# Kernel optimization log

Hardware: AMD Instinct MI355X
Metric: run time of the kernel (lower is better)

## Reference

```python
import jax, jax.numpy as jnp
import numpy as np

BN_EPS = 1e-3      # Keras BatchNormalization default epsilon
LRELU_ALPHA = 0.3  # Keras LeakyReLU default alpha


def _bn(x, gamma, beta, mean, var):
    # inference-mode batch norm over the feature (last) axis
    return gamma * (x - mean) * jax.lax.rsqrt(var + BN_EPS) + beta


def _gcn(x, adj, w, b):
    # spektral GCNConv: A_hat @ (X @ W) + b   (adj assumed pre-normalized)
    xw = jnp.einsum('bnf,fc->bnc', x, w)
    return jnp.einsum('bnm,bmc->bnc', adj, xw) + b


def _lrelu(x):
    return jnp.where(x >= 0, x, LRELU_ALPHA * x)


def setup_inputs() -> dict:
    key = jax.random.key(0)
    ks = jax.random.split(key, 12)
    B, N, C = 16, 1024, 256
    x = jax.random.normal(ks[0], (B, N, C), dtype=jnp.float32)
    # roughly row-normalized dense adjacency (stands in for D^-1/2 (A+I) D^-1/2)
    adj = jax.random.uniform(ks[1], (B, N, N), dtype=jnp.float32) / N
    s = 1.0 / np.sqrt(C)
    return {
        'x': x,
        'adj': adj,
        'bn1_gamma': jnp.ones((C,), jnp.float32),
        'bn1_beta': jnp.zeros((C,), jnp.float32),
        'bn1_mean': jax.random.normal(ks[2], (C,), jnp.float32) * 0.1,
        'bn1_var': jax.random.uniform(ks[3], (C,), jnp.float32) + 0.5,
        'w1': jax.random.normal(ks[4], (C, C), jnp.float32) * s,
        'b1': jnp.zeros((C,), jnp.float32),
        'bn2_gamma': jnp.ones((C,), jnp.float32),
        'bn2_beta': jnp.zeros((C,), jnp.float32),
        'bn2_mean': jax.random.normal(ks[5], (C,), jnp.float32) * 0.1,
        'bn2_var': jax.random.uniform(ks[6], (C,), jnp.float32) + 0.5,
        'w2': jax.random.normal(ks[7], (C, C), jnp.float32) * s,
        'b2': jnp.zeros((C,), jnp.float32),
        'w_skip': jax.random.normal(ks[8], (C, C), jnp.float32) * s,
        'b_skip': jnp.zeros((C,), jnp.float32),
    }


def reference(x, adj, bn1_gamma, bn1_beta, bn1_mean, bn1_var, w1, b1,
              bn2_gamma, bn2_beta, bn2_mean, bn2_var, w2, b2, w_skip, b_skip):
    h = _bn(x, bn1_gamma, bn1_beta, bn1_mean, bn1_var)          # BN(input)
    out = _lrelu(_gcn(h, adj, w1, b1))                          # GCNConv + LeakyReLU
    out = _bn(out, bn2_gamma, bn2_beta, bn2_mean, bn2_var)      # BN
    out = _lrelu(_gcn(out, adj, w2, b2))                        # GCNConv + LeakyReLU
    skip = _gcn(h, adj, w_skip, b_skip)                         # skip GCNConv on BN(input)
    # Dropout is identity at inference
    return out + skip
```

## Files before the change

kernel.cpp:

```cpp
#include <hip/hip_runtime.h>

#define LRELU_ALPHA 0.3f
#define BN_EPS 1e-3f

using u16 = unsigned short;
using u32 = unsigned int;

typedef __attribute__((ext_vector_type(8))) short bf16x8;
typedef __attribute__((ext_vector_type(4))) float f32x4;

struct alignas(8) U16x4 { u16 x, y, z, w; };

__device__ __forceinline__ u16 f2bf(float f) {
  union { float f; u32 u; } v; v.f = f;
  u32 b = v.u;
  b += 0x7FFFu + ((b >> 16) & 1u);
  return (u16)(b >> 16);
}
__device__ __forceinline__ float bf2f(u16 h) {
  union { u32 u; float f; } v; v.u = ((u32)h) << 16;
  return v.f;
}

typedef const __attribute__((address_space(1))) void* gas_ptr;
typedef __attribute__((address_space(3))) void* las_ptr;

__device__ __forceinline__ void gload16(const void* g, void* l) {
  __builtin_amdgcn_global_load_lds((gas_ptr)g, (las_ptr)l, 16, 0, 0);
}

__device__ __forceinline__ int xcd_swz512(int lid) {
  return (lid & 7) * 64 + (lid >> 3);
}

template <int K>
__device__ __forceinline__ void gemm_core(const u16* __restrict__ A,
                                          const u16* __restrict__ B,
                                          u16* lds, f32x4 (&acc)[4][4]) {
  const int t = threadIdx.x, lane = t & 63, wid = t >> 6;
  const int wm = (wid >> 1) * 64, wn = (wid & 1) * 64;
  const int lrow = lane & 15, lk = (lane >> 4) * 8;
  const int r0 = t >> 3, ce = (t & 7) * 8, lo = wid * 512;
  u16* ldsA = lds;
  u16* ldsB = lds + 8192;
#pragma unroll 1
  for (int kt = 0; kt < K / 64; ++kt) {
    const u16* gA = A + kt * 64;
    const u16* gB = B + kt * 64;
#pragma unroll
    for (int cc = 0; cc < 4; ++cc) {
      gload16(gA + (size_t)(cc * 32 + r0) * K + ce, ldsA + cc * 2048 + lo);
      gload16(gB + (size_t)(cc * 32 + r0) * K + ce, ldsB + cc * 2048 + lo);
    }
    asm volatile("s_waitcnt vmcnt(0)" ::: "memory");
    __syncthreads();
#pragma unroll
    for (int kk = 0; kk < 2; ++kk) {
      bf16x8 a[4], b[4];
#pragma unroll
      for (int i = 0; i < 4; ++i)
        a[i] = *(const bf16x8*)(ldsA + (wm + i * 16 + lrow) * 64 + kk * 32 + lk);
#pragma unroll
      for (int i = 0; i < 4; ++i)
        b[i] = *(const bf16x8*)(ldsB + (wn + i * 16 + lrow) * 64 + kk * 32 + lk);
#pragma unroll
      for (int i = 0; i < 4; ++i)
#pragma unroll
        for (int j = 0; j < 4; ++j)
          acc[i][j] = __builtin_amdgcn_mfma_f32_16x16x32_bf16(a[i], b[j], acc[i][j], 0, 0, 0);
    }
    __syncthreads();
  }
}

template <int K>
__device__ __forceinline__ void gemm_core64(const u16* __restrict__ A,
                                            const u16* __restrict__ B,
                                            u16* lds, f32x4 (&acc)[2][4]) {
  const int t = threadIdx.x, lane = t & 63, wid = t >> 6;
  const int wm = wid * 32;
  const int lrow = lane & 15, lk = (lane >> 4) * 8;
  const int r0 = t >> 3, ce = (t & 7) * 8, lo = wid * 512;
  u16* ldsA = lds;
  u16* ldsB = lds + 8192;
#pragma unroll 1
  for (int kt = 0; kt < K / 64; ++kt) {
    const u16* gA = A + kt * 64;
    const u16* gB = B + kt * 64;
#pragma unroll
    for (int cc = 0; cc < 4; ++cc)
      gload16(gA + (size_t)(cc * 32 + r0) * K + ce, ldsA + cc * 2048 + lo);
#pragma unroll
    for (int cc = 0; cc < 2; ++cc)
      gload16(gB + (size_t)(cc * 32 + r0) * K + ce, ldsB + cc * 2048 + lo);
    asm volatile("s_waitcnt vmcnt(0)" ::: "memory");
    __syncthreads();
#pragma unroll
    for (int kk = 0; kk < 2; ++kk) {
      bf16x8 a[2], b[4];
#pragma unroll
      for (int i = 0; i < 2; ++i)
        a[i] = *(const bf16x8*)(ldsA + (wm + i * 16 + lrow) * 64 + kk * 32 + lk);
#pragma unroll
      for (int j = 0; j < 4; ++j)
        b[j] = *(const bf16x8*)(ldsB + (j * 16 + lrow) * 64 + kk * 32 + lk);
#pragma unroll
      for (int i = 0; i < 2; ++i)
#pragma unroll
        for (int j = 0; j < 4; ++j)
          acc[i][j] = __builtin_amdgcn_mfma_f32_16x16x32_bf16(a[i], b[j], acc[i][j], 0, 0, 0);
    }
    __syncthreads();
  }
}

#define ACC_INIT(R)                                 \
  f32x4 acc[R][4];                                  \
  _Pragma("unroll") for (int i_ = 0; i_ < R; ++i_)  \
  _Pragma("unroll") for (int j_ = 0; j_ < 4; ++j_)  \
      acc[i_][j_] = {0.f, 0.f, 0.f, 0.f};

__global__ __launch_bounds__(256) void k_prep_h(
    const float* __restrict__ w1, const float* __restrict__ wsk, const float* __restrict__ w2,
    const float* __restrict__ g1, const float* __restrict__ be1,
    const float* __restrict__ m1, const float* __restrict__ v1,
    const float* __restrict__ g2, const float* __restrict__ be2,
    const float* __restrict__ m2, const float* __restrict__ v2,
    const float* __restrict__ x,
    u16* __restrict__ wcatT, u16* __restrict__ w2T,
    float* __restrict__ s2, float* __restrict__ t2c, u16* __restrict__ h_bf) {
  int bid = blockIdx.x;
  if (bid < 768) {
    if (bid == 0) {
      int c = threadIdx.x;
      float a2 = g2[c] * rsqrtf(v2[c] + BN_EPS);
      s2[c] = a2;
      t2c[c] = be2[c] - m2[c] * a2;
    }
    int i = bid * 256 + threadIdx.x;
    if (i < 131072) {
      int co = i >> 8, ci = i & 255;
      const float* w = (co < 256) ? w1 : wsk;
      wcatT[i] = f2bf(w[ci * 256 + (co & 255)]);
    } else {
      int k = i - 131072;
      int co = k >> 8, ci = k & 255;
      w2T[k] = f2bf(w2[ci * 256 + co]);
    }
  } else {
    int base = (bid - 768) * 256 + threadIdx.x;
    int c0 = (base << 2) & 255;
    float sc[4], sh[4];
#pragma unroll
    for (int u = 0; u < 4; ++u) {
      int c = c0 + u;
      float a = g1[c] * rsqrtf(v1[c] + BN_EPS);
      sc[u] = a;
      sh[u] = be1[c] - m1[c] * a;
    }
#pragma unroll
    for (int j = 0; j < 16; ++j) {
      int k = j * 65536 + base;
      float4 v = ((const float4*)x)[k];
      U16x4 o = {f2bf(v.x * sc[0] + sh[0]), f2bf(v.y * sc[1] + sh[1]),
                 f2bf(v.z * sc[2] + sh[2]), f2bf(v.w * sc[3] + sh[3])};
      ((U16x4*)h_bf)[k] = o;
    }
  }
}

__global__ __launch_bounds__(256) void k_cvt(const float* __restrict__ adj,
                                             u16* __restrict__ adj_bf) {
  const int N4 = 4194304;
  int stride = gridDim.x * blockDim.x;
  for (int idx = blockIdx.x * blockDim.x + threadIdx.x; idx < N4; idx += stride) {
    float4 v = ((const float4*)adj)[idx];
    U16x4 o = {f2bf(v.x), f2bf(v.y), f2bf(v.z), f2bf(v.w)};
    ((U16x4*)adj_bf)[idx] = o;
  }
}

__global__ __launch_bounds__(256) void k_xw(const u16* __restrict__ h_bf,
                                            const u16* __restrict__ wcatT,
                                            u16* __restrict__ hwT) {
  __shared__ u16 lds[17408];
  const int wg = xcd_swz512(blockIdx.x);
  const int mt = wg >> 2, nt = wg & 3;
  ACC_INIT(4);
  gemm_core<256>(h_bf + (size_t)mt * 128 * 256, wcatT + (size_t)nt * 128 * 256, lds, acc);

  const int t = threadIdx.x, lane = t & 63, wid = t >> 6;
  const int row0 = (wid >> 1) * 64 + (lane >> 4) * 4;
  const int col0 = (wid & 1) * 64 + (lane & 15);
  __syncthreads();
  u16* tl = lds;
#pragma unroll
  for (int j = 0; j < 4; ++j) {
    int co_l = col0 + j * 16;
#pragma unroll
    for (int i = 0; i < 4; ++i)
#pragma unroll
      for (int q = 0; q < 4; ++q)
        tl[co_l * 136 + row0 + i * 16 + q] = f2bf(acc[i][j][q]);
  }
  __syncthreads();
  const int rw = t >> 4, seg = t & 15;
  const int b = mt >> 3, nb = (mt & 7) * 128;
#pragma unroll
  for (int p = 0; p < 8; ++p) {
    int co_l = p * 16 + rw;
    *(bf16x8*)(hwT + (((size_t)(b * 512 + nt * 128 + co_l)) << 10) + nb + seg * 8) =
        *(const bf16x8*)(tl + co_l * 136 + seg * 8);
  }
}

__global__ __launch_bounds__(256) void k_big1(const u16* __restrict__ adj_bf,
                                              const u16* __restrict__ hwT,
                                              const float* __restrict__ b1,
                                              const float* __restrict__ bsk,
                                              const float* __restrict__ s2,
                                              const float* __restrict__ t2c,
                                              u16* __restrict__ u2b,
                                              u16* __restrict__ skipb) {
  __shared__ u16 lds[17408];
  ACC_INIT(4);
  const int wg = xcd_swz512(blockIdx.x);
  const int mt = wg & 7, nt = (wg >> 3) & 3, bz = wg >> 5;
  gemm_core<1024>(adj_bf + ((size_t)bz << 20) + (size_t)mt * 128 * 1024,
                  hwT    + ((size_t)bz << 19) + (size_t)nt * 128 * 1024, lds, acc);

  const int t = threadIdx.x, lane = t & 63, wid = t >> 6;
  const int row0 = (wid >> 1) * 64 + (lane >> 4) * 4;
  const int col0 = (wid & 1) * 64 + (lane & 15);
  const bool conv = (nt < 2);
  const int cb = (nt & 1) * 128;
  __syncthreads();
  u16* tl = lds;
#pragma unroll
  for (int j = 0; j < 4; ++j) {
    int cl = col0 + j * 16;
    int c = cb + cl;
    float bias = conv ? b1[c] : bsk[c];
    float sc = s2[c], tc = t2c[c];
#pragma unroll
    for (int i = 0; i < 4; ++i)
#pragma unroll
      for (int q = 0; q < 4; ++q) {
        float y = acc[i][j][q] + bias;
        float v;
        if (conv) {
          float u = (y >= 0.f) ? y : LRELU_ALPHA * y;
          v = fmaf(u, sc, tc);
        } else {
          v = y;
        }
        tl[(row0 + i * 16 + q) * 136 + cl] = f2bf(v);
      }
  }
  __syncthreads();
  u16* dstbase = (conv ? u2b : skipb) + ((size_t)bz << 18) + cb;
  const int rw = t >> 4, seg = t & 15;
  const int nb = mt * 128;
#pragma unroll
  for (int p = 0; p < 8; ++p) {
    int nl = p * 16 + rw;
    *(bf16x8*)(dstbase + ((size_t)(nb + nl) << 8) + seg * 8) =
        *(const bf16x8*)(tl + nl * 136 + seg * 8);
  }
}

__global__ __launch_bounds__(256) void k_sm2(const u16* __restrict__ w2T,
                                             const u16* __restrict__ u2b,
                                             u16* __restrict__ t2T) {
  __shared__ u16 lds[12288];
  ACC_INIT(2);
  const int mt = blockIdx.x, nt = blockIdx.y, bz = blockIdx.z;
  gemm_core64<256>(w2T + (size_t)mt * 128 * 256,
                   u2b + ((size_t)bz << 18) + (size_t)nt * 64 * 256, lds, acc);

  const int t = threadIdx.x, lane = t & 63, wid = t >> 6;
  const int row0 = wid * 32 + (lane >> 4) * 4;
  const int col0 = lane & 15;
  __syncthreads();
  u16* tl = lds;
#pragma unroll
  for (int j = 0; j < 4; ++j)
#pragma unroll
    for (int i = 0; i < 2; ++i)
#pragma unroll
      for (int q = 0; q < 4; ++q)
        tl[(row0 + i * 16 + q) * 72 + col0 + j * 16] = f2bf(acc[i][j][q]);
  __syncthreads();
  u16* base = t2T + ((size_t)bz << 18) + nt * 64;
  const int rw = t >> 3, seg = t & 7;
#pragma unroll
  for (int p = 0; p < 4; ++p) {
    int co = p * 32 + rw;
    *(bf16x8*)(base + (((size_t)(mt * 128 + co)) << 10) + seg * 8) =
        *(const bf16x8*)(tl + co * 72 + seg * 8);
  }
}

__global__ __launch_bounds__(256) void k_big2(const u16* __restrict__ adj_bf,
                                              const u16* __restrict__ t2T,
                                              const float* __restrict__ b2,
                                              const u16* __restrict__ skipb,
                                              float* __restrict__ outp) {
  __shared__ u16 lds[17408];
  ACC_INIT(2);
  const int wg = xcd_swz512(blockIdx.x);
  const int mt = wg & 7, nt = (wg >> 3) & 3, bz = wg >> 5;
  gemm_core64<1024>(adj_bf + ((size_t)bz << 20) + (size_t)mt * 128 * 1024,
                    t2T    + ((size_t)bz << 18) + (size_t)nt * 64 * 1024, lds, acc);

  const int t = threadIdx.x, lane = t & 63, wid = t >> 6;
  const int row0 = wid * 32 + (lane >> 4) * 4;
  const int col0 = lane & 15;
  __syncthreads();
  float* tf = (float*)lds;
#pragma unroll
  for (int j = 0; j < 4; ++j) {
    int cl = col0 + j * 16;
    float bias = b2[nt * 64 + cl];
#pragma unroll
    for (int i = 0; i < 2; ++i)
#pragma unroll
      for (int q = 0; q < 4; ++q) {
        float y = acc[i][j][q] + bias;
        tf[(row0 + i * 16 + q) * 68 + cl] = (y >= 0.f) ? y : LRELU_ALPHA * y;
      }
  }
  __syncthreads();
  const int rw = t >> 4, seg = t & 15;
#pragma unroll
  for (int p = 0; p < 8; ++p) {
    int nl = p * 16 + rw;
    size_t go = ((size_t)bz << 18) + ((size_t)(mt * 128 + nl) << 8) + nt * 64 + seg * 4;
    float4 v = *(const float4*)(tf + nl * 68 + seg * 4);
    U16x4 sk = *(const U16x4*)(skipb + go);
    float4 o = {v.x + bf2f(sk.x), v.y + bf2f(sk.y), v.z + bf2f(sk.z), v.w + bf2f(sk.w)};
    *(float4*)(outp + go) = o;
  }
}

extern "C" void kernel_launch(void* const* d_in, const int* in_sizes, int n_in,
                              void* d_out, int out_size, void* d_ws, size_t ws_size,
                              hipStream_t stream) {
  const float* x   = (const float*)d_in[0];
  const float* adj = (const float*)d_in[1];
  const float* g1  = (const float*)d_in[2];
  const float* be1 = (const float*)d_in[3];
  const float* mu1 = (const float*)d_in[4];
  const float* v1  = (const float*)d_in[5];
  const float* w1  = (const float*)d_in[6];
  const float* b1  = (const float*)d_in[7];
  const float* g2  = (const float*)d_in[8];
  const float* be2 = (const float*)d_in[9];
  const float* mu2 = (const float*)d_in[10];
  const float* v2  = (const float*)d_in[11];
  const float* w2  = (const float*)d_in[12];
  const float* b2  = (const float*)d_in[13];
  const float* wsk = (const float*)d_in[14];
  const float* bsk = (const float*)d_in[15];
  float* out = (float*)d_out;

  char* ws = (char*)d_ws;
  u16*   adj_bf = (u16*)(ws);
  u16*   hwT    = (u16*)(ws + 33554432);
  u16*   h_bf   = (u16*)(ws + 50331648);
  u16*   u2b    = (u16*)(ws + 58720256);
  u16*   t2T    = (u16*)(ws + 67108864);
  u16*   skipb  = (u16*)(ws + 75497472);
  u16*   wcatT  = (u16*)(ws + 83886080);
  u16*   w2T    = (u16*)(ws + 84148224);
  float* s2     = (float*)(ws + 84281344);
  float* t2c    = (float*)(ws + 84282368);
  if (ws_size < 84283392) return;

  k_prep_h <<<1024, 256, 0, stream>>>(w1, wsk, w2, g1, be1, mu1, v1, g2, be2, mu2, v2,
                                      x, wcatT, w2T, s2, t2c, h_bf);
  k_cvt    <<<2048, 256, 0, stream>>>(adj, adj_bf);
  k_xw     <<<512,  256, 0, stream>>>(h_bf, wcatT, hwT);
  k_big1   <<<512,  256, 0, stream>>>(adj_bf, hwT, b1, bsk, s2, t2c, u2b, skipb);
  k_sm2 <<<dim3(2, 16, 16), 256, 0, stream>>>(w2T, u2b, t2T);
  k_big2   <<<512,  256, 0, stream>>>(adj_bf, t2T, b2, skipb, out);
}
```

Baseline: 210.7 us.

## Move skip GCN aggregation into second adjacency GEMM and merge conversion kernels

The skip branch's adjacency product is removed from k_big1, which now computes only the conv half with 64-wide tiles. It is instead computed inside k_big2 through a dual-B GEMM core that shares each loaded adj tile across both t2T and the skip columns of hwT. This drops the bf16 skipb intermediate's write and read, and the skip result is kept in fp32 until the final add. The adj fp32-to-bf16 conversion is also folded into the prep kernel, removing one launch. In exchange k_big2 carries two accumulator sets, which raises register pressure and may lower occupancy.

```diff
diff --git a/kernel.cpp b/kernel.cpp
--- a/kernel.cpp
+++ b/kernel.cpp
@@ -114,21 +114,73 @@
   }
 }
 
-#define ACC_INIT(R)                                 \
-  f32x4 acc[R][4];                                  \
-  _Pragma("unroll") for (int i_ = 0; i_ < R; ++i_)  \
-  _Pragma("unroll") for (int j_ = 0; j_ < 4; ++j_)  \
-      acc[i_][j_] = {0.f, 0.f, 0.f, 0.f};
-
-__global__ __launch_bounds__(256) void k_prep_h(
+template <int K>
+__device__ __forceinline__ void gemm_core64x2(const u16* __restrict__ A,
+                                              const u16* __restrict__ B1,
+                                              const u16* __restrict__ B2,
+                                              u16* lds, f32x4 (&acc1)[2][4],
+                                              f32x4 (&acc2)[2][4]) {
+  const int t = threadIdx.x, lane = t & 63, wid = t >> 6;
+  const int wm = wid * 32;
+  const int lrow = lane & 15, lk = (lane >> 4) * 8;
+  const int r0 = t >> 3, ce = (t & 7) * 8, lo = wid * 512;
+  u16* ldsA  = lds;
+  u16* ldsB1 = lds + 8192;
+  u16* ldsB2 = lds + 12288;
+#pragma unroll 1
+  for (int kt = 0; kt < K / 64; ++kt) {
+    const u16* gA  = A  + kt * 64;
+    const u16* gB1 = B1 + kt * 64;
+    const u16* gB2 = B2 + kt * 64;
+#pragma unroll
+    for (int cc = 0; cc < 4; ++cc)
+      gload16(gA + (size_t)(cc * 32 + r0) * K + ce, ldsA + cc * 2048 + lo);
+#pragma unroll
+    for (int cc = 0; cc < 2; ++cc) {
+      gload16(gB1 + (size_t)(cc * 32 + r0) * K + ce, ldsB1 + cc * 2048 + lo);
+      gload16(gB2 + (size_t)(cc * 32 + r0) * K + ce, ldsB2 + cc * 2048 + lo);
+    }
+    asm volatile("s_waitcnt vmcnt(0)" ::: "memory");
+    __syncthreads();
+#pragma unroll
+    for (int kk = 0; kk < 2; ++kk) {
+      bf16x8 a[2], b1[4], b2[4];
+#pragma unroll
+      for (int i = 0; i < 2; ++i)
+        a[i] = *(const bf16x8*)(ldsA + (wm + i * 16 + lrow) * 64 + kk * 32 + lk);
+#pragma unroll
+      for (int j = 0; j < 4; ++j) {
+        b1[j] = *(const bf16x8*)(ldsB1 + (j * 16 + lrow) * 64 + kk * 32 + lk);
+        b2[j] = *(const bf16x8*)(ldsB2 + (j * 16 + lrow) * 64 + kk * 32 + lk);
+      }
+#pragma unroll
+      for (int i = 0; i < 2; ++i)
+#pragma unroll
+        for (int j = 0; j < 4; ++j) {
+          acc1[i][j] = __builtin_amdgcn_mfma_f32_16x16x32_bf16(a[i], b1[j], acc1[i][j], 0, 0, 0);
+          acc2[i][j] = __builtin_amdgcn_mfma_f32_16x16x32_bf16(a[i], b2[j], acc2[i][j], 0, 0, 0);
+        }
+    }
+    __syncthreads();
+  }
+}
+
+#define ACC_INIT_N(name, R)                          \
+  f32x4 name[R][4];                                  \
+  _Pragma("unroll") for (int i_ = 0; i_ < R; ++i_)   \
+  _Pragma("unroll") for (int j_ = 0; j_ < 4; ++j_)   \
+      name[i_][j_] = {0.f, 0.f, 0.f, 0.f};
+
+__global__ __launch_bounds__(256) void k_pre(
     const float* __restrict__ w1, const float* __restrict__ wsk, const float* __restrict__ w2,
     const float* __restrict__ g1, const float* __restrict__ be1,
     const float* __restrict__ m1, const float* __restrict__ v1,
     const float* __restrict__ g2, const float* __restrict__ be2,
     const float* __restrict__ m2, const float* __restrict__ v2,
-    const float* __restrict__ x,
+    const float* __restrict__ x, const float* __restrict__ adj,
     u16* __restrict__ wcatT, u16* __restrict__ w2T,
-    float* __restrict__ s2, float* __restrict__ t2c, u16* __restrict__ h_bf) {
+    float* __restrict__ s2, float* __restrict__ t2c,
+    u16* __restrict__ h_bf, u16* __restrict__ adj_bf) {
   int bid = blockIdx.x;
   if (bid < 768) {
     if (bid == 0) {
@@ -147,7 +199,7 @@
       int co = k >> 8, ci = k & 255;
       w2T[k] = f2bf(w2[ci * 256 + co]);
     }
-  } else {
+  } else if (bid < 1024) {
     int base = (bid - 768) * 256 + threadIdx.x;
     int c0 = (base << 2) & 255;
     float sc[4], sh[4];
@@ -166,17 +218,16 @@
                  f2bf(v.z * sc[2] + sh[2]), f2bf(v.w * sc[3] + sh[3])};
       ((U16x4*)h_bf)[k] = o;
     }
-  }
-}
-
-__global__ __launch_bounds__(256) void k_cvt(const float* __restrict__ adj,
-                                             u16* __restrict__ adj_bf) {
-  const int N4 = 4194304;
-  int stride = gridDim.x * blockDim.x;
-  for (int idx = blockIdx.x * blockDim.x + threadIdx.x; idx < N4; idx += stride) {
-    float4 v = ((const float4*)adj)[idx];
-    U16x4 o = {f2bf(v.x), f2bf(v.y), f2bf(v.z), f2bf(v.w)};
-    ((U16x4*)adj_bf)[idx] = o;
+  } else {
+    const int N4 = 4194304;
+    int idx = (bid - 1024) * 256 + threadIdx.x;
+    const int stride = 2048 * 256;
+#pragma unroll 1
+    for (; idx < N4; idx += stride) {
+      float4 v = ((const float4*)adj)[idx];
+      U16x4 o = {f2bf(v.x), f2bf(v.y), f2bf(v.z), f2bf(v.w)};
+      ((U16x4*)adj_bf)[idx] = o;
+    }
   }
 }
 
@@ -186,7 +237,7 @@
   __shared__ u16 lds[17408];
   const int wg = xcd_swz512(blockIdx.x);
   const int mt = wg >> 2, nt = wg & 3;
-  ACC_INIT(4);
+  ACC_INIT_N(acc, 4);
   gemm_core<256>(h_bf + (size_t)mt * 128 * 256, wcatT + (size_t)nt * 128 * 256, lds, acc);
 
   const int t = threadIdx.x, lane = t & 63, wid = t >> 6;
@@ -217,55 +268,43 @@
 __global__ __launch_bounds__(256) void k_big1(const u16* __restrict__ adj_bf,
                                               const u16* __restrict__ hwT,
                                               const float* __restrict__ b1,
-                                              const float* __restrict__ bsk,
                                               const float* __restrict__ s2,
                                               const float* __restrict__ t2c,
-                                              u16* __restrict__ u2b,
-                                              u16* __restrict__ skipb) {
+                                              u16* __restrict__ u2b) {
   __shared__ u16 lds[17408];
-  ACC_INIT(4);
+  ACC_INIT_N(acc, 2);
   const int wg = xcd_swz512(blockIdx.x);
   const int mt = wg & 7, nt = (wg >> 3) & 3, bz = wg >> 5;
-  gemm_core<1024>(adj_bf + ((size_t)bz << 20) + (size_t)mt * 128 * 1024,
-                  hwT    + ((size_t)bz << 19) + (size_t)nt * 128 * 1024, lds, acc);
-
-  const int t = threadIdx.x, lane = t & 63, wid = t >> 6;
-  const int row0 = (wid >> 1) * 64 + (lane >> 4) * 4;
-  const int col0 = (wid & 1) * 64 + (lane & 15);
-  const bool conv = (nt < 2);
-  const int cb = (nt & 1) * 128;
+  gemm_core64<1024>(adj_bf + ((size_t)bz << 20) + (size_t)mt * 128 * 1024,
+                    hwT    + ((size_t)bz << 19) + ((size_t)(nt * 64) << 10), lds, acc);
+
+  const int t = threadIdx.x, lane = t & 63, wid = t >> 6;
+  const int row0 = wid * 32 + (lane >> 4) * 4;
+  const int col0 = lane & 15;
   __syncthreads();
   u16* tl = lds;
 #pragma unroll
   for (int j = 0; j < 4; ++j) {
     int cl = col0 + j * 16;
-    int c = cb + cl;
-    float bias = conv ? b1[c] : bsk[c];
-    float sc = s2[c], tc = t2c[c];
-#pragma unroll
-    for (int i = 0; i < 4; ++i)
+    int c = nt * 64 + cl;
+    float bias = b1[c], sc = s2[c], tc = t2c[c];
+#pragma unroll
+    for (int i = 0; i < 2; ++i)
 #pragma unroll
       for (int q = 0; q < 4; ++q) {
         float y = acc[i][j][q] + bias;
-        float v;
-        if (conv) {
-          float u = (y >= 0.f) ? y : LRELU_ALPHA * y;
-          v = fmaf(u, sc, tc);
-        } else {
-          v = y;
-        }
-        tl[(row0 + i * 16 + q) * 136 + cl] = f2bf(v);
+        float u = (y >= 0.f) ? y : LRELU_ALPHA * y;
+        tl[(row0 + i * 16 + q) * 72 + cl] = f2bf(fmaf(u, sc, tc));
       }
   }
   __syncthreads();
-  u16* dstbase = (conv ? u2b : skipb) + ((size_t)bz << 18) + cb;
-  const int rw = t >> 4, seg = t & 15;
-  const int nb = mt * 128;
-#pragma unroll
-  for (int p = 0; p < 8; ++p) {
-    int nl = p * 16 + rw;
-    *(bf16x8*)(dstbase + ((size_t)(nb + nl) << 8) + seg * 8) =
-        *(const bf16x8*)(tl + nl * 136 + seg * 8);
+  u16* dstbase = u2b + ((size_t)bz << 18) + nt * 64;
+  const int rw = t >> 3, seg = t & 7;
+#pragma unroll
+  for (int p = 0; p < 4; ++p) {
+    int nl = p * 32 + rw;
+    *(bf16x8*)(dstbase + ((size_t)(mt * 128 + nl) << 8) + seg * 8) =
+        *(const bf16x8*)(tl + nl * 72 + seg * 8);
   }
 }
 
@@ -273,7 +312,7 @@
                                              const u16* __restrict__ u2b,
                                              u16* __restrict__ t2T) {
   __shared__ u16 lds[12288];
-  ACC_INIT(2);
+  ACC_INIT_N(acc, 2);
   const int mt = blockIdx.x, nt = blockIdx.y, bz = blockIdx.z;
   gemm_core64<256>(w2T + (size_t)mt * 128 * 256,
                    u2b + ((size_t)bz << 18) + (size_t)nt * 64 * 256, lds, acc);
@@ -303,15 +342,19 @@
 
 __global__ __launch_bounds__(256) void k_big2(const u16* __restrict__ adj_bf,
                                               const u16* __restrict__ t2T,
+                                              const u16* __restrict__ hwT,
                                               const float* __restrict__ b2,
-                                              const u16* __restrict__ skipb,
+                                              const float* __restrict__ bsk,
                                               float* __restrict__ outp) {
   __shared__ u16 lds[17408];
-  ACC_INIT(2);
+  ACC_INIT_N(acc1, 2);
+  ACC_INIT_N(acc2, 2);
   const int wg = xcd_swz512(blockIdx.x);
   const int mt = wg & 7, nt = (wg >> 3) & 3, bz = wg >> 5;
-  gemm_core64<1024>(adj_bf + ((size_t)bz << 20) + (size_t)mt * 128 * 1024,
-                    t2T    + ((size_t)bz << 18) + (size_t)nt * 64 * 1024, lds, acc);
+  gemm_core64x2<1024>(adj_bf + ((size_t)bz << 20) + (size_t)mt * 128 * 1024,
+                      t2T    + ((size_t)bz << 18) + ((size_t)(nt * 64) << 10),
+                      hwT    + ((size_t)bz << 19) + ((size_t)(256 + nt * 64) << 10),
+                      lds, acc1, acc2);
 
   const int t = threadIdx.x, lane = t & 63, wid = t >> 6;
   const int row0 = wid * 32 + (lane >> 4) * 4;
@@ -321,13 +364,15 @@
 #pragma unroll
   for (int j = 0; j < 4; ++j) {
     int cl = col0 + j * 16;
-    float bias = b2[nt * 64 + cl];
+    int c = nt * 64 + cl;
+    float bc = b2[c], bs = bsk[c];
 #pragma unroll
     for (int i = 0; i < 2; ++i)
 #pragma unroll
       for (int q = 0; q < 4; ++q) {
-        float y = acc[i][j][q] + bias;
-        tf[(row0 + i * 16 + q) * 68 + cl] = (y >= 0.f) ? y : LRELU_ALPHA * y;
+        float y = acc1[i][j][q] + bc;
+        float conv = (y >= 0.f) ? y : LRELU_ALPHA * y;
+        tf[(row0 + i * 16 + q) * 68 + cl] = conv + acc2[i][j][q] + bs;
       }
   }
   __syncthreads();
@@ -336,10 +381,7 @@
   for (int p = 0; p < 8; ++p) {
     int nl = p * 16 + rw;
     size_t go = ((size_t)bz << 18) + ((size_t)(mt * 128 + nl) << 8) + nt * 64 + seg * 4;
-    float4 v = *(const float4*)(tf + nl * 68 + seg * 4);
-    U16x4 sk = *(const U16x4*)(skipb + go);
-    float4 o = {v.x + bf2f(sk.x), v.y + bf2f(sk.y), v.z + bf2f(sk.z), v.w + bf2f(sk.w)};
-    *(float4*)(outp + go) = o;
+    *(float4*)(outp + go) = *(const float4*)(tf + nl * 68 + seg * 4);
   }
 }
 
@@ -370,18 +412,16 @@
   u16*   h_bf   = (u16*)(ws + 50331648);
   u16*   u2b    = (u16*)(ws + 58720256);
   u16*   t2T    = (u16*)(ws + 67108864);
-  u16*   skipb  = (u16*)(ws + 75497472);
   u16*   wcatT  = (u16*)(ws + 83886080);
   u16*   w2T    = (u16*)(ws + 84148224);
   float* s2     = (float*)(ws + 84281344);
   float* t2c    = (float*)(ws + 84282368);
   if (ws_size < 84283392) return;
 
-  k_prep_h <<<1024, 256, 0, stream>>>(w1, wsk, w2, g1, be1, mu1, v1, g2, be2, mu2, v2,
-                                      x, wcatT, w2T, s2, t2c, h_bf);
-  k_cvt    <<<2048, 256, 0, stream>>>(adj, adj_bf);
-  k_xw     <<<512,  256, 0, stream>>>(h_bf, wcatT, hwT);
-  k_big1   <<<512,  256, 0, stream>>>(adj_bf, hwT, b1, bsk, s2, t2c, u2b, skipb);
-  k_sm2 <<<dim3(2, 16, 16), 256, 0, stream>>>(w2T, u2b, t2T);
-  k_big2   <<<512,  256, 0, stream>>>(adj_bf, t2T, b2, skipb, out);
-}
+  k_pre  <<<3072, 256, 0, stream>>>(w1, wsk, w2, g1, be1, mu1, v1, g2, be2, mu2, v2,
+                                    x, adj, wcatT, w2T, s2, t2c, h_bf, adj_bf);
+  k_xw   <<<512,  256, 0, stream>>>(h_bf, wcatT, hwT);
+  k_big1 <<<512,  256, 0, stream>>>(adj_bf, hwT, b1, s2, t2c, u2b);
+  k_sm2  <<<dim3(2, 16, 16), 256, 0, stream>>>(w2T, u2b, t2T);
+  k_big2 <<<512,  256, 0, stream>>>(adj_bf, t2T, hwT, b2, bsk, out);
+}
```

Result: faster. 205.4 us (-2.5%).
